# Performance work log

Hardware: AMD Instinct MI355X
Metric: run time of the kernel (lower is better)

## Reference

```python
import jax, jax.numpy as jnp
import numpy as np

T, D, TR, CC, L = 4096, 512, 64, 64, 3  # time, input_size, trace, context, num_blocks


def setup_inputs() -> dict:
    key = jax.random.key(0)
    ks = jax.random.split(key, 10)
    x = jax.random.normal(ks[0], (T, D), dtype=jnp.float32)
    state = jnp.zeros((L, 1, TR, CC), dtype=jnp.float32)  # initial recurrent state (real part; imag is 0)
    start = jax.random.uniform(ks[1], (T,)) < 0.02  # episode-reset mask
    Wtr = jax.random.normal(ks[2], (L, TR, D), dtype=jnp.float32) / np.float32(np.sqrt(D))
    Wc = jax.random.normal(ks[3], (L, TR, D), dtype=jnp.float32) / np.float32(np.sqrt(D))
    a = jax.random.uniform(ks[4], (L, TR), minval=1e-6, maxval=0.1)
    b = 2 * jnp.pi / jnp.exp(jax.random.uniform(ks[5], (L, CC), minval=0.0, maxval=float(np.log(10000.0))))
    F = 2 * TR * CC
    W0 = jax.random.normal(ks[6], (L, D, F), dtype=jnp.float32) * np.float32(0.01 / np.sqrt(F))  # default_init scale=0.01
    b0 = jnp.zeros((L, D)); g0 = jnp.ones((L, D)); beta0 = jnp.zeros((L, D))
    W1 = jax.random.normal(ks[7], (L, D, D), dtype=jnp.float32) / np.float32(np.sqrt(D))
    b1 = jnp.zeros((L, D)); g1 = jnp.ones((L, D)); beta1 = jnp.zeros((L, D))
    return dict(x=x, state=state, start=start, Wtr=Wtr, Wc=Wc, a=a, b=b,
                W0=W0, b0=b0, g0=g0, beta0=beta0, W1=W1, b1=b1, g1=g1, beta1=beta1)


def _layernorm(z, g, b):
    m = jnp.mean(z, axis=-1, keepdims=True)
    v = jnp.mean((z - m) ** 2, axis=-1, keepdims=True)
    return (z - m) / jnp.sqrt(v + 1e-5) * g + b


def _sffm(x, st0, start, Wtr, Wc, a, b, W0, b0, g0, bb0, W1, b1, g1, bb1):
    t_len = x.shape[0]
    tr = x @ Wtr.T           # [T, TR]
    ct = x @ Wc.T            # [T, CC] (context proj also has trace_size outputs)
    pre = jnp.abs(tr[:, :, None] * ct[:, None, :])            # [T, TR, CC]
    pre = pre / (1e-8 + jnp.sum(pre, axis=(-2, -1), keepdims=True))
    # complex decay per (trace, context) pair: exp((-|a| + i b) * dt)
    ab = (-jnp.abs(a))[:, None] + 1j * b[None, :]             # [TR, CC] complex64

    def combine(carry, inc):
        ps, s, i = carry
        st, xx, j = inc
        s = s * jnp.logical_not(st)                            # reset gating
        dt = (j - i).astype(jnp.float32)[:, None, None]
        new = s * jnp.exp(ab[None] * dt) + xx
        return (jnp.logical_or(st, ps), new, j)

    ts = jnp.arange(t_len + 1, dtype=jnp.int32)
    sb = jnp.concatenate([jnp.zeros((1, 1, 1), bool), start.reshape(t_len, 1, 1)], axis=0)
    xs = jnp.concatenate([st0.astype(jnp.complex64), pre.astype(jnp.complex64)], axis=0)
    _, ns, _ = jax.lax.associative_scan(combine, (sb, xs, ts), axis=0)
    ns = ns[1:]                                                # [T, TR, CC] complex

    s = ns.reshape(t_len, TR * CC)
    mag = jnp.log1p(jnp.abs(s))
    ang = jnp.angle(s)
    scaled = jnp.concatenate([mag * jnp.sin(ang), mag * jnp.cos(ang)], axis=-1)  # [T, 2*TR*CC]
    z = jax.nn.leaky_relu(_layernorm(scaled @ W0.T + b0, g0, bb0))
    z = jax.nn.leaky_relu(_layernorm(z @ W1.T + b1, g1, bb1))
    return z


def reference(x, state, start, Wtr, Wc, a, b, W0, b0, g0, beta0, W1, b1, g1, beta1):
    z = x
    for l in range(L):
        z = _sffm(x, state[l], start, Wtr[l], Wc[l], a[l], b[l],
                  W0[l], b0[l], g0[l], beta0[l], W1[l], b1[l], g1[l], beta1[l])
        x = x + z
    return z  # NSFFM returns the last block's y
```

## Files before the change

### kernel.cpp

```cpp
#include <hip/hip_runtime.h>
#include <hip/hip_bf16.h>
#include <math.h>

#define T_LEN 4096
#define D_DIM 512
#define F_DIM 8192
#define NCHUNK 64
#define CLEN 64

typedef short short8 __attribute__((ext_vector_type(8)));
typedef float f32x4 __attribute__((ext_vector_type(4)));
typedef unsigned short u16;
typedef unsigned int u32;

__device__ inline float wave_sum(float v) {
#pragma unroll
  for (int o = 32; o; o >>= 1) v += __shfl_xor(v, o);
  return v;
}

__device__ inline u16 f2bf_bits(float v) {
  __hip_bfloat16 h = __float2bfloat16(v);
  return *(u16*)&h;
}

__device__ inline float bf2f(u16 u) {
  u32 x = ((u32)u) << 16;
  return *(float*)&x;
}

__device__ inline void gl_lds16(const void* g, void* l) {
  __builtin_amdgcn_global_load_lds((const __attribute__((address_space(1))) void*)g,
                                   (__attribute__((address_space(3))) void*)l, 16, 0, 0);
}

__global__ void detect_start(const unsigned char* __restrict__ s8, int* __restrict__ mode) {
  __shared__ int found;
  if (threadIdx.x == 0) found = 0;
  __syncthreads();
  for (int i = threadIdx.x; i < 4096; i += 256)
    if ((i & 3) && s8[i]) found = 1;
  __syncthreads();
  if (threadIdx.x == 0) mode[0] = found;
}

__device__ inline int read_start(const unsigned char* s8, const int* s32, int mode, int t) {
  return mode ? (int)s8[t] : s32[t];
}

__global__ void f2bf(const float* __restrict__ s, u16* __restrict__ d, int n) {
  int i = blockIdx.x * 256 + threadIdx.x;
  if (i < n) d[i] = f2bf_bits(s[i]);
}

__global__ void k_conv(const float* __restrict__ wtr, const float* __restrict__ wc,
                       u16* __restrict__ wcat, const float* __restrict__ w0,
                       u16* __restrict__ w0bf) {
  int i = blockIdx.x * 256 + threadIdx.x;
  if (i < 128 * D_DIM) {
    float v = (i < 64 * D_DIM) ? wtr[i] : wc[i - 64 * D_DIM];
    wcat[i] = f2bf_bits(v);
  }
  int j = i - 128 * D_DIM;
  if (j >= 0 && j < D_DIM * F_DIM) {
    int d = j >> 13, f = j & 8191;
    int r = f >> 7, rem = f & 127;
    int c = rem >> 1, b = rem & 1;
    float v = w0[(size_t)d * 8192 + b * 4096 + r * 64 + c];
    w0bf[(size_t)d * 8192 + (f ^ ((d & 7) << 3))] = f2bf_bits(v);
  }
}

template <int BM, int BN, int WR, int WC>
__global__ __launch_bounds__(256) void gemm_bt(const u16* __restrict__ A,
                                               const u16* __restrict__ B,
                                               float* __restrict__ C, int M, int N, int K) {
  constexpr int BK = 32;
  constexpr int MT = BM / (WR * 16);
  constexpr int NT = BN / (WC * 16);
  constexpr int AG = BM / 64;
  constexpr int BG = BN / 64;
  __shared__ u16 sA[BM * BK];
  __shared__ u16 sB[BN * BK];
  const int m0 = blockIdx.x * BM;
  const int n0 = blockIdx.y * BN;
  const int tid = threadIdx.x;
  const int wave = tid >> 6;
  const int lane = tid & 63;
  const int wr = wave / WC;
  const int wc = wave % WC;
  const int row_l = tid >> 2;
  const int c8 = (tid & 3) << 3;
  const int frow = lane & 15;
  const int fcol = (lane >> 4) << 3;

  f32x4 acc[MT][NT];
#pragma unroll
  for (int i = 0; i < MT; ++i)
#pragma unroll
    for (int j = 0; j < NT; ++j) acc[i][j] = (f32x4){0.f, 0.f, 0.f, 0.f};

  for (int k0 = 0; k0 < K; k0 += BK) {
#pragma unroll
    for (int j = 0; j < AG; ++j) {
      uint4 v = *(const uint4*)(A + (size_t)(m0 + j * 64 + row_l) * K + (k0 + c8));
      *(uint4*)(sA + (j * 64 + row_l) * BK + c8) = v;
    }
#pragma unroll
    for (int j = 0; j < BG; ++j) {
      uint4 v = *(const uint4*)(B + (size_t)(n0 + j * 64 + row_l) * K + (k0 + c8));
      *(uint4*)(sB + (j * 64 + row_l) * BK + c8) = v;
    }
    __syncthreads();
    short8 af[MT], bfr[NT];
#pragma unroll
    for (int i = 0; i < MT; ++i)
      af[i] = *(const short8*)(sA + (wr * MT * 16 + i * 16 + frow) * BK + fcol);
#pragma unroll
    for (int j = 0; j < NT; ++j)
      bfr[j] = *(const short8*)(sB + (wc * NT * 16 + j * 16 + frow) * BK + fcol);
#pragma unroll
    for (int i = 0; i < MT; ++i)
#pragma unroll
      for (int j = 0; j < NT; ++j)
        acc[i][j] = __builtin_amdgcn_mfma_f32_16x16x32_bf16(af[i], bfr[j], acc[i][j], 0, 0, 0);
    __syncthreads();
  }
#pragma unroll
  for (int i = 0; i < MT; ++i) {
    const int rbase = m0 + wr * MT * 16 + i * 16 + ((lane >> 4) << 2);
#pragma unroll
    for (int j = 0; j < NT; ++j) {
      const int col = n0 + wc * NT * 16 + j * 16 + (lane & 15);
#pragma unroll
      for (int rg = 0; rg < 4; ++rg) C[(size_t)(rbase + rg) * N + col] = acc[i][j][rg];
    }
  }
}

__global__ __launch_bounds__(256) void gemm128(const u16* __restrict__ A,
                                               const u16* __restrict__ B,
                                               u16* __restrict__ Cp, size_t pstride, int N,
                                               int Ktot) {
  __shared__ u16 sA[128 * 64];
  __shared__ u16 sB[128 * 64];
  const int tid = threadIdx.x;
  const int wave = tid >> 6;
  const int lane = tid & 63;
  const int wr = wave >> 1;
  const int wc = wave & 1;
  const int m0 = blockIdx.x * 128;
  const int n0 = blockIdx.y * 128;
  const int ks = blockIdx.z;
  const int Kper = Ktot / gridDim.z;
  const int kb = ks * Kper;
  const int row_s = tid >> 3;
  const int g8 = (tid & 7) << 3;
  const int frow = lane & 15;
  const int quad = lane >> 4;
  const int sw = frow & 7;

  f32x4 acc[4][4];
#pragma unroll
  for (int i = 0; i < 4; ++i)
#pragma unroll
    for (int j = 0; j < 4; ++j) acc[i][j] = (f32x4){0.f, 0.f, 0.f, 0.f};

  for (int k0 = kb; k0 < kb + Kper; k0 += 64) {
#pragma unroll
    for (int j = 0; j < 4; ++j) {
      gl_lds16(A + (size_t)(m0 + j * 32 + row_s) * Ktot + (k0 + g8), sA + j * 2048 + wave * 512);
      gl_lds16(B + (size_t)(n0 + j * 32 + row_s) * Ktot + (k0 + g8), sB + j * 2048 + wave * 512);
    }
    asm volatile("s_waitcnt vmcnt(0)" ::: "memory");
    __syncthreads();
#pragma unroll
    for (int kk = 0; kk < 2; ++kk) {
      const int gA = (((kk << 2) | quad) ^ sw) << 3;
      short8 af[4], bfr[4];
#pragma unroll
      for (int i = 0; i < 4; ++i)
        af[i] = *(const short8*)(sA + (wr * 64 + i * 16 + frow) * 64 + gA);
#pragma unroll
      for (int j = 0; j < 4; ++j)
        bfr[j] = *(const short8*)(sB + (wc * 64 + j * 16 + frow) * 64 + gA);
#pragma unroll
      for (int i = 0; i < 4; ++i)
#pragma unroll
        for (int j = 0; j < 4; ++j)
          acc[i][j] = __builtin_amdgcn_mfma_f32_16x16x32_bf16(af[i], bfr[j], acc[i][j], 0, 0, 0);
    }
    __syncthreads();
  }
#pragma unroll
  for (int i = 0; i < 4; ++i) {
    const int rbase = m0 + wr * 64 + i * 16 + ((lane >> 4) << 2);
#pragma unroll
    for (int j = 0; j < 4; ++j) {
      const int col = n0 + wc * 64 + j * 16 + (lane & 15);
#pragma unroll
      for (int rg = 0; rg < 4; ++rg)
        Cp[(size_t)ks * pstride + (size_t)(rbase + rg) * N + col] = f2bf_bits(acc[i][j][rg]);
    }
  }
}

__global__ void prep_pq(const float* __restrict__ trct, float* __restrict__ pT,
                        float* __restrict__ q) {
  int t = blockIdx.x;
  int lane = threadIdx.x;
  float tr = trct[t * 128 + lane];
  float ct = trct[t * 128 + 64 + lane];
  float ap = fabsf(tr), aq = fabsf(ct);
  float Sp = wave_sum(ap);
  float Sq = wave_sum(aq);
  float denom = 1e-8f + Sp * Sq;
  pT[lane * T_LEN + t] = ap;
  q[t * 64 + lane] = aq / denom;
}

__global__ void scan_phase1(const float* __restrict__ pT, const float* __restrict__ q,
                            const unsigned char* __restrict__ st8, const int* __restrict__ st32,
                            const int* __restrict__ modep, const float* __restrict__ a,
                            const float* __restrict__ b, float4* __restrict__ chunkbuf) {
  int chunk = blockIdx.x, r = blockIdx.y, c = threadIdx.x;
  int mode = modep[0];
  int t0 = chunk * CLEN;
  float na = -fabsf(a[r]);
  float rho = __expf(na);
  float bb = b[c];
  float er = rho * __cosf(bb), ei = rho * __sinf(bb);
  float pv = pT[r * T_LEN + t0 + c];
  int sv = read_start(st8, st32, mode, t0 + c);
  unsigned long long bal = __ballot(sv != 0);
  float Ar, Ai;
  if (bal) {
    Ar = 0.f; Ai = 0.f;
  } else {
    float mag = __expf(64.f * na);
    float ang = 64.f * bb;
    Ar = mag * __cosf(ang);
    Ai = mag * __sinf(ang);
  }
  int L = bal ? (63 - __builtin_clzll(bal)) : 0;
  float Br = 0.f, Bi = 0.f;
  const float* qrow = q + (size_t)t0 * 64 + c;
  for (int i = L; i < CLEN; ++i) {
    float pre = __shfl(pv, i) * qrow[i * 64];
    float nBr = er * Br - ei * Bi + pre;
    Bi = er * Bi + ei * Br;
    Br = nBr;
  }
  chunkbuf[((size_t)chunk * 64 + r) * 64 + c] = make_float4(Ar, Ai, Br, Bi);
}

__global__ void scan_phase2(const float4* __restrict__ chunkbuf, const float* __restrict__ state,
                            float2* __restrict__ s0buf) {
  int r = blockIdx.x, c = threadIdx.x;
  float Sr = state[r * 64 + c], Si = 0.f;
  for (int k = 0; k < NCHUNK; ++k) {
    s0buf[((size_t)k * 64 + r) * 64 + c] = make_float2(Sr, Si);
    float4 ab = chunkbuf[((size_t)k * 64 + r) * 64 + c];
    float nSr = ab.x * Sr - ab.y * Si + ab.z;
    Si = ab.x * Si + ab.y * Sr + ab.w;
    Sr = nSr;
  }
}

__global__ void scan_phase3(const float* __restrict__ pT, const float* __restrict__ q,
                            const unsigned char* __restrict__ st8, const int* __restrict__ st32,
                            const int* __restrict__ modep, const float* __restrict__ a,
                            const float* __restrict__ b, const float2* __restrict__ s0buf,
                            u32* __restrict__ scaled, int c0) {
  int chunk = c0 + blockIdx.x, r = blockIdx.y, c = threadIdx.x;
  int mode = modep[0];
  int t0 = chunk * CLEN;
  float rho = __expf(-fabsf(a[r]));
  float bb = b[c];
  float er = rho * __cosf(bb), ei = rho * __sinf(bb);
  float pv = pT[r * T_LEN + t0 + c];
  int sv = read_start(st8, st32, mode, t0 + c);
  float2 s0 = s0buf[((size_t)chunk * 64 + r) * 64 + c];
  float Sr = s0.x, Si = s0.y;
  int tl0 = (chunk - c0) * CLEN;
  const float* qrow = q + (size_t)t0 * 64 + c;
  u32* srow = scaled + (size_t)tl0 * 4096;
  const int Ldw = r * 64 + c;
#pragma unroll 4
  for (int i = 0; i < CLEN; ++i) {
    float qt = qrow[i * 64];
    float pt = __shfl(pv, i);
    int st = __shfl(sv, i);
    float pre = pt * qt;
    float cer = st ? 0.f : er;
    float cei = st ? 0.f : ei;
    float nSr = cer * Sr - cei * Si + pre;
    Si = cer * Si + cei * Sr;
    Sr = nSr;
    float m2 = fmaf(Sr, Sr, Si * Si);
    float rsq = rsqrtf(fmaxf(m2, 1e-30f));
    float m = m2 * rsq;
    float sc = __log2f(1.0f + m) * 0.6931471805599453f * rsq;
    u32 pack = ((u32)f2bf_bits(sc * Sr) << 16) | (u32)f2bf_bits(sc * Si);
    srow[(size_t)i * 4096 + (Ldw ^ ((i & 7) << 2))] = pack;
  }
}

__global__ void ln_act16(const u16* __restrict__ parts, int KS, size_t pstride,
                         const float* __restrict__ bias, const float* __restrict__ gam,
                         const float* __restrict__ bet, u16* __restrict__ zbf) {
  __shared__ float red[8];
  int t = blockIdx.x, tid = threadIdx.x;
  size_t o = (size_t)t * D_DIM + tid;
  float v0 = bias[tid];
  float v1 = bias[tid + 256];
  for (int ks = 0; ks < KS; ++ks) {
    v0 += bf2f(parts[(size_t)ks * pstride + o]);
    v1 += bf2f(parts[(size_t)ks * pstride + o + 256]);
  }
  float s = wave_sum(v0 + v1);
  if ((tid & 63) == 0) red[tid >> 6] = s;
  __syncthreads();
  float mean = (red[0] + red[1] + red[2] + red[3]) * (1.f / 512.f);
  float d0 = v0 - mean, d1 = v1 - mean;
  float s2 = wave_sum(d0 * d0 + d1 * d1);
  if ((tid & 63) == 0) red[4 + (tid >> 6)] = s2;
  __syncthreads();
  float var = (red[4] + red[5] + red[6] + red[7]) * (1.f / 512.f);
  float rstd = rsqrtf(var + 1e-5f);
  float z0 = d0 * rstd * gam[tid] + bet[tid];
  float z1 = d1 * rstd * gam[tid + 256] + bet[tid + 256];
  z0 = z0 > 0.f ? z0 : 0.01f * z0;
  z1 = z1 > 0.f ? z1 : 0.01f * z1;
  zbf[o] = f2bf_bits(z0);
  zbf[o + 256] = f2bf_bits(z1);
}

__global__ void ln_act32(const float* __restrict__ y, const float* __restrict__ bias,
                         const float* __restrict__ gam, const float* __restrict__ bet,
                         const float* __restrict__ xsrc, float* __restrict__ xdst,
                         u16* __restrict__ xbf_next, float* __restrict__ finout) {
  __shared__ float red[8];
  int t = blockIdx.x, tid = threadIdx.x;
  size_t o = (size_t)t * D_DIM + tid;
  float v0 = y[o] + bias[tid];
  float v1 = y[o + 256] + bias[tid + 256];
  float s = wave_sum(v0 + v1);
  if ((tid & 63) == 0) red[tid >> 6] = s;
  __syncthreads();
  float mean = (red[0] + red[1] + red[2] + red[3]) * (1.f / 512.f);
  float d0 = v0 - mean, d1 = v1 - mean;
  float s2 = wave_sum(d0 * d0 + d1 * d1);
  if ((tid & 63) == 0) red[4 + (tid >> 6)] = s2;
  __syncthreads();
  float var = (red[4] + red[5] + red[6] + red[7]) * (1.f / 512.f);
  float rstd = rsqrtf(var + 1e-5f);
  float z0 = d0 * rstd * gam[tid] + bet[tid];
  float z1 = d1 * rstd * gam[tid + 256] + bet[tid + 256];
  z0 = z0 > 0.f ? z0 : 0.01f * z0;
  z1 = z1 > 0.f ? z1 : 0.01f * z1;
  if (xdst) {
    float x0 = xsrc[o] + z0, x1 = xsrc[o + 256] + z1;
    xdst[o] = x0;
    xdst[o + 256] = x1;
    xbf_next[o] = f2bf_bits(x0);
    xbf_next[o + 256] = f2bf_bits(x1);
  }
  if (finout) {
    finout[o] = z0;
    finout[o + 256] = z1;
  }
}

__global__ void err_signal(float* __restrict__ out, float code) {
  if (threadIdx.x == 0) out[0] = code;
}

extern "C" void kernel_launch(void* const* d_in, const int* in_sizes, int n_in, void* d_out,
                              int out_size, void* d_ws, size_t ws_size, hipStream_t stream) {
  const float* x_in = (const float*)d_in[0];
  const float* state = (const float*)d_in[1];
  const unsigned char* start8 = (const unsigned char*)d_in[2];
  const int* start32 = (const int*)d_in[2];
  const float* Wtr = (const float*)d_in[3];
  const float* Wc = (const float*)d_in[4];
  const float* a_in = (const float*)d_in[5];
  const float* b_in = (const float*)d_in[6];
  const float* W0 = (const float*)d_in[7];
  const float* b0 = (const float*)d_in[8];
  const float* g0 = (const float*)d_in[9];
  const float* beta0 = (const float*)d_in[10];
  const float* W1 = (const float*)d_in[11];
  const float* b1 = (const float*)d_in[12];
  const float* g1 = (const float*)d_in[13];
  const float* beta1 = (const float*)d_in[14];
  float* out = (float*)d_out;

  char* w = (char*)d_ws;
  auto alloc = [&](size_t bytes) {
    char* ptr = w;
    w += (bytes + 255) & ~(size_t)255;
    return ptr;
  };
  float* x_ws = (float*)alloc(4ull * T_LEN * D_DIM);
  u16* xbf = (u16*)alloc(2ull * T_LEN * D_DIM);
  u16* wcat = (u16*)alloc(2ull * 128 * D_DIM);
  u16* w0bf = (u16*)alloc(2ull * D_DIM * F_DIM);
  u16* w1bf = (u16*)alloc(2ull * 3 * D_DIM * D_DIM);
  float* trct = (float*)alloc(4ull * T_LEN * 128);
  float* pTbuf = (float*)alloc(4ull * T_LEN * 64);
  float* qbuf = (float*)alloc(4ull * T_LEN * 64);
  float4* chunkbuf = (float4*)alloc(16ull * NCHUNK * 64 * 64);
  float2* s0buf = (float2*)alloc(8ull * NCHUNK * 64 * 64);
  u16* z0bf = (u16*)alloc(2ull * T_LEN * D_DIM);
  float* ybuf = (float*)alloc(4ull * T_LEN * D_DIM);
  int* modep = (int*)alloc(256);
  size_t base1 = (size_t)(w - (char*)d_ws);

  if (n_in != 15) {
    err_signal<<<1, 64, 0, stream>>>(out, 9e6f + 1000.f * n_in);
    return;
  }
  const size_t MB = 1ull << 20;
  const size_t pstride = (size_t)T_LEN * D_DIM;
  int KS, nseg;
  if (ws_size >= base1 + 16 * MB + 64 * MB) { KS = 4; nseg = 1; }
  else if (ws_size >= base1 + 16 * MB + 32 * MB) { KS = 4; nseg = 2; }
  else if (ws_size >= base1 + 8 * MB + 32 * MB) { KS = 2; nseg = 2; }
  else if (ws_size >= base1 + 8 * MB + 16 * MB) { KS = 2; nseg = 4; }
  else if (ws_size >= base1 + 4 * MB + 16 * MB) { KS = 1; nseg = 4; }
  else {
    err_signal<<<1, 64, 0, stream>>>(out, 9e6f);
    return;
  }
  const int seg_rows = T_LEN / nseg;
  const int seg_chunks = NCHUNK / nseg;
  u16* ypart = (u16*)alloc(2ull * KS * pstride);
  u16* scaled = (u16*)alloc(2ull * seg_rows * F_DIM);

  detect_start<<<1, 256, 0, stream>>>(start8, modep);
  f2bf<<<(T_LEN * D_DIM) / 256, 256, 0, stream>>>(x_in, xbf, T_LEN * D_DIM);
  f2bf<<<(3 * D_DIM * D_DIM) / 256, 256, 0, stream>>>(W1, w1bf, 3 * D_DIM * D_DIM);

  for (int l = 0; l < 3; ++l) {
    const float* Wtr_l = Wtr + (size_t)l * 64 * D_DIM;
    const float* Wc_l = Wc + (size_t)l * 64 * D_DIM;
    const float* a_l = a_in + l * 64;
    const float* b_l = b_in + l * 64;
    const float* W0_l = W0 + (size_t)l * D_DIM * F_DIM;
    const u16* w1bf_l = w1bf + (size_t)l * D_DIM * D_DIM;
    const float* state_l = state + (size_t)l * 64 * 64;
    const float* xsrc = (l == 0) ? x_in : x_ws;

    k_conv<<<(128 * D_DIM + D_DIM * F_DIM) / 256, 256, 0, stream>>>(Wtr_l, Wc_l, wcat, W0_l,
                                                                    w0bf);
    gemm_bt<64, 64, 2, 2><<<dim3(T_LEN / 64, 2), 256, 0, stream>>>(xbf, wcat, trct, T_LEN, 128,
                                                                   D_DIM);
    prep_pq<<<T_LEN, 64, 0, stream>>>(trct, pTbuf, qbuf);
    scan_phase1<<<dim3(NCHUNK, 64), 64, 0, stream>>>(pTbuf, qbuf, start8, start32, modep, a_l,
                                                     b_l, chunkbuf);
    scan_phase2<<<64, 64, 0, stream>>>(chunkbuf, state_l, s0buf);

    for (int h = 0; h < nseg; ++h) {
      scan_phase3<<<dim3(seg_chunks, 64), 64, 0, stream>>>(pTbuf, qbuf, start8, start32, modep,
                                                           a_l, b_l, s0buf, (u32*)scaled,
                                                           h * seg_chunks);
      gemm128<<<dim3(seg_rows / 128, D_DIM / 128, KS), 256, 0, stream>>>(
          scaled, w0bf, ypart + (size_t)h * seg_rows * D_DIM, pstride, D_DIM, F_DIM);
    }
    ln_act16<<<T_LEN, 256, 0, stream>>>(ypart, KS, pstride, b0 + l * D_DIM, g0 + l * D_DIM,
                                        beta0 + l * D_DIM, z0bf);
    gemm_bt<64, 64, 2, 2><<<dim3(T_LEN / 64, D_DIM / 64), 256, 0, stream>>>(z0bf, w1bf_l, ybuf,
                                                                            T_LEN, D_DIM, D_DIM);
    ln_act32<<<T_LEN, 256, 0, stream>>>(ybuf, b1 + l * D_DIM, g1 + l * D_DIM, beta1 + l * D_DIM,
                                        (l < 2) ? xsrc : nullptr, (l < 2) ? x_ws : nullptr,
                                        (l < 2) ? xbf : nullptr, (l == 2) ? out : nullptr);
  }
}
```

Before: 516.9 us.

## Add 8-phase pipelined 256x128 MFMA GEMM for the scaled x W0 projection

Adds a new GEMM kernel with 512 threads, 256x128 output tiles and 96 KB of dynamic LDS. It double-buffers A and B tiles and splits each 128-wide K step into eight phases, interleaving async global-to-LDS loads with MFMA work and raising wave priority around the MFMA blocks. It is used for the large scaled x W0 GEMM when the workspace allows a single segment and the shared-memory attribute can be set. The aim is to hide memory latency and improve data reuse, at the cost of higher LDS use and fragile hand-placed waitcnt and barrier ordering.

```diff
diff --git a/kernel.cpp b/kernel.cpp
--- a/kernel.cpp
+++ b/kernel.cpp
@@ -198,6 +198,128 @@
 #pragma unroll
     for (int j = 0; j < 4; ++j) {
       const int col = n0 + wc * 64 + j * 16 + (lane & 15);
+#pragma unroll
+      for (int rg = 0; rg < 4; ++rg)
+        Cp[(size_t)ks * pstride + (size_t)(rbase + rg) * N + col] = f2bf_bits(acc[i][j][rg]);
+    }
+  }
+}
+
+__global__ __launch_bounds__(512, 2) void gemm_8ph(const u16* __restrict__ A,
+                                                   const u16* __restrict__ B,
+                                                   u16* __restrict__ Cp, size_t pstride, int N,
+                                                   int Ktot) {
+  extern __shared__ u16 smem[];
+  u16* sA = smem;
+  u16* sB = smem + 32768;
+  const int tid = threadIdx.x;
+  const int wave = tid >> 6;
+  const int lane = tid & 63;
+  const int wr = wave >> 2;
+  const int wc = wave & 3;
+  const int m0 = blockIdx.x * 256;
+  const int n0 = blockIdx.y * 128;
+  const int ks = blockIdx.z;
+  const int Kper = Ktot / gridDim.z;
+  const int kb = ks * Kper;
+  const int NITER = Kper >> 7;
+  const int r_l = tid >> 3;
+  const int g8 = (tid & 7) << 3;
+  const int frow = lane & 15;
+  const int quad = lane >> 4;
+  const int sw = frow & 7;
+
+  const u16* Abase = A + (size_t)(m0 + r_l) * Ktot + g8;
+  const u16* Bbase = B + (size_t)(n0 + r_l) * Ktot + g8;
+
+#define STAGE_A(l, k0, b) \
+  gl_lds16(Abase + (size_t)(l) * 64 * Ktot + (k0), sA + (b)*16384 + (l)*4096 + wave * 512)
+#define STAGE_B(l, k0, b) \
+  gl_lds16(Bbase + (size_t)(l) * 64 * Ktot + (k0), sB + (b)*8192 + (l)*4096 + wave * 512)
+
+  f32x4 acc[8][2];
+#pragma unroll
+  for (int i = 0; i < 8; ++i) {
+    acc[i][0] = (f32x4){0.f, 0.f, 0.f, 0.f};
+    acc[i][1] = (f32x4){0.f, 0.f, 0.f, 0.f};
+  }
+
+  STAGE_A(0, kb, 0);
+  STAGE_A(1, kb, 0);
+  STAGE_A(2, kb, 0);
+  STAGE_A(3, kb, 0);
+  STAGE_B(0, kb, 0);
+  STAGE_B(1, kb, 0);
+  STAGE_A(0, kb + 64, 1);
+  STAGE_A(2, kb + 64, 1);
+  asm volatile("s_waitcnt vmcnt(2)" ::: "memory");
+  __builtin_amdgcn_s_barrier();
+
+  short8 af[4][2];
+  short8 bfc[2][2];
+
+  for (int I = 0; I < NITER; ++I) {
+    const int k0e = kb + (I << 7);
+    const bool nl = (I < NITER - 1);
+#pragma unroll
+    for (int p = 0; p < 8; ++p) {
+      const int b = p >> 2;
+      const int qr = (p >> 1) & 1;
+      const int qc = p & 1;
+      if (qc == 0) {
+#pragma unroll
+        for (int f = 0; f < 4; ++f)
+#pragma unroll
+          for (int kk = 0; kk < 2; ++kk)
+            af[f][kk] = *(const short8*)(sA + b * 16384 +
+                                         (wr * 128 + (qr * 4 + f) * 16 + frow) * 64 +
+                                         ((((kk << 2) | quad) ^ sw) << 3));
+      }
+      if (p == 0 || p == 4) {
+#pragma unroll
+        for (int fc = 0; fc < 2; ++fc)
+#pragma unroll
+          for (int kk = 0; kk < 2; ++kk)
+            bfc[fc][kk] = *(const short8*)(sB + b * 8192 + (wc * 32 + fc * 16 + frow) * 64 +
+                                           ((((kk << 2) | quad) ^ sw) << 3));
+      }
+      if (p == 0) { STAGE_A(1, k0e + 64, 1); STAGE_A(3, k0e + 64, 1); }
+      if (p == 1) { STAGE_B(0, k0e + 64, 1); STAGE_B(1, k0e + 64, 1); }
+      if (p == 3 && nl) { STAGE_A(0, k0e + 128, 0); STAGE_A(2, k0e + 128, 0); }
+      if (p == 4 && nl) { STAGE_A(1, k0e + 128, 0); STAGE_A(3, k0e + 128, 0); }
+      if (p == 5 && nl) { STAGE_B(0, k0e + 128, 0); STAGE_B(1, k0e + 128, 0); }
+      if (p == 7 && nl) { STAGE_A(0, k0e + 192, 1); STAGE_A(2, k0e + 192, 1); }
+      __builtin_amdgcn_s_barrier();
+      asm volatile("s_waitcnt lgkmcnt(0)" ::: "memory");
+      __builtin_amdgcn_sched_barrier(0);
+      __builtin_amdgcn_s_setprio(1);
+#pragma unroll
+      for (int f = 0; f < 4; ++f)
+#pragma unroll
+        for (int kk = 0; kk < 2; ++kk)
+          acc[qr * 4 + f][qc] =
+              __builtin_amdgcn_mfma_f32_16x16x32_bf16(af[f][kk], bfc[qc][kk], acc[qr * 4 + f][qc],
+                                                      0, 0, 0);
+      __builtin_amdgcn_s_setprio(0);
+      if (p == 3) {
+        if (nl)
+          asm volatile("s_waitcnt vmcnt(2)" ::: "memory");
+        else
+          asm volatile("s_waitcnt vmcnt(0)" ::: "memory");
+      }
+      if (p == 7 && nl) asm volatile("s_waitcnt vmcnt(2)" ::: "memory");
+      __builtin_amdgcn_s_barrier();
+    }
+  }
+#undef STAGE_A
+#undef STAGE_B
+
+#pragma unroll
+  for (int i = 0; i < 8; ++i) {
+    const int rbase = m0 + wr * 128 + i * 16 + (quad << 2);
+#pragma unroll
+    for (int j = 0; j < 2; ++j) {
+      const int col = n0 + wc * 32 + j * 16 + frow;
 #pragma unroll
       for (int rg = 0; rg < 4; ++rg)
         Cp[(size_t)ks * pstride + (size_t)(rbase + rg) * N + col] = f2bf_bits(acc[i][j][rg]);
@@ -396,6 +518,15 @@
   const float* beta1 = (const float*)d_in[14];
   float* out = (float*)d_out;
 
+  static int attr_state = 0;
+  if (attr_state == 0)
+    attr_state = (hipFuncSetAttribute((const void*)gemm_8ph,
+                                      hipFuncAttributeMaxDynamicSharedMemorySize,
+                                      98304) == hipSuccess)
+                     ? 1
+                     : -1;
+  const bool attr_ok = (attr_state == 1);
+
   char* w = (char*)d_ws;
   auto alloc = [&](size_t bytes) {
     char* ptr = w;
@@ -438,6 +569,8 @@
   u16* ypart = (u16*)alloc(2ull * KS * pstride);
   u16* scaled = (u16*)alloc(2ull * seg_rows * F_DIM);
 
+  const bool use8 = (nseg == 1) && attr_ok;
+
   detect_start<<<1, 256, 0, stream>>>(start8, modep);
   f2bf<<<(T_LEN * D_DIM) / 256, 256, 0, stream>>>(x_in, xbf, T_LEN * D_DIM);
   f2bf<<<(3 * D_DIM * D_DIM) / 256, 256, 0, stream>>>(W1, w1bf, 3 * D_DIM * D_DIM);
@@ -465,8 +598,12 @@
       scan_phase3<<<dim3(seg_chunks, 64), 64, 0, stream>>>(pTbuf, qbuf, start8, start32, modep,
                                                            a_l, b_l, s0buf, (u32*)scaled,
                                                            h * seg_chunks);
-      gemm128<<<dim3(seg_rows / 128, D_DIM / 128, KS), 256, 0, stream>>>(
-          scaled, w0bf, ypart + (size_t)h * seg_rows * D_DIM, pstride, D_DIM, F_DIM);
+      if (use8)
+        gemm_8ph<<<dim3(seg_rows / 256, D_DIM / 128, KS), 512, 98304, stream>>>(
+            scaled, w0bf, ypart + (size_t)h * seg_rows * D_DIM, pstride, D_DIM, F_DIM);
+      else
+        gemm128<<<dim3(seg_rows / 128, D_DIM / 128, KS), 256, 0, stream>>>(
+            scaled, w0bf, ypart + (size_t)h * seg_rows * D_DIM, pstride, D_DIM, F_DIM);
     }
     ln_act16<<<T_LEN, 256, 0, stream>>>(ypart, KS, pstride, b0 + l * D_DIM, g0 + l * D_DIM,
                                         beta0 + l * D_DIM, z0bf);
```

After: 495.8 us. 1.04x faster.
